# Kernel optimization log

Measured on AMD Instinct MI355X. Metric: run time of the kernel, lower is better.

## Reference

```python
import jax, jax.numpy as jnp
import numpy as np

# MoEFeedForward from ViziMarketTransformer (h100_moe_preset dims), eval mode (dropout = identity).
D, F, E, K = 512, 2048, 8, 2   # d_model, d_ff, n_experts, top_k
B, T = 8, 4096
AUX_W = 0.01


def setup_inputs() -> dict:
    key = jax.random.key(0)
    k0, k1, k2, k3 = jax.random.split(key, 4)
    s_in = 1.0 / np.sqrt(D)
    s_mid = 1.0 / np.sqrt(F)
    return {
        "x": jax.random.normal(k0, (B, T, D), jnp.float32),
        "router_w": (jax.random.normal(k1, (D, E), jnp.float32) * s_in),   # nn.Linear(d_model, n_experts, bias=False)
        "w1": (jax.random.normal(k2, (E, D, F), jnp.float32) * s_in),      # per-expert Linear(d_model, d_ff)
        "b1": jnp.zeros((E, F), jnp.float32),
        "w2": (jax.random.normal(k3, (E, F, D), jnp.float32) * s_mid),     # per-expert Linear(d_ff, d_model)
        "b2": jnp.zeros((E, D), jnp.float32),
    }


def reference(x, router_w, w1, b1, w2, b2):
    Bb, Tt, Dd = x.shape
    xf = x.reshape(-1, Dd)                                   # (N, D), N = B*T
    logits = xf @ router_w                                   # (N, E)
    topk_vals, topk_idx = jax.lax.top_k(logits, K)           # (N, K)
    topk_w = jax.nn.softmax(topk_vals, axis=-1)              # (N, K)
    # Combine weights per expert: sum over k of softmax weight where topk_idx == e.
    comb = jnp.sum(jax.nn.one_hot(topk_idx, E, dtype=xf.dtype) * topk_w[..., None], axis=1)  # (N, E)
    out = jnp.zeros_like(xf)
    for e in range(E):  # small fixed expert count; tokens fully vectorized
        h = jax.nn.gelu(xf @ w1[e] + b1[e], approximate=False)   # exact GELU, as nn.GELU()
        out = out + comb[:, e:e + 1] * (h @ w2[e] + b2[e])
    # Switch/GShard auxiliary load-balancing loss.
    probs = jax.nn.softmax(logits, axis=-1)
    avg_prob = probs.mean(axis=0)                             # (E,)
    avg_frac = jax.nn.one_hot(topk_idx[:, 0], E, dtype=xf.dtype).mean(axis=0)  # (E,)
    aux_loss = AUX_W * E * jnp.sum(avg_prob * avg_frac)
    return out.reshape(Bb, Tt, Dd), aux_loss
```

## Files before the change

### kernel.cpp

```cpp
#include <hip/hip_runtime.h>
#include <hip/hip_fp16.h>
#include <cstdint>
#include <cstddef>

#define NTOK 32768
#define DM 512
#define FF 2048
#define NE 8
#define BM 128
#define FBLK 128
#define NFB (FF / FBLK)

typedef _Float16 half8 __attribute__((ext_vector_type(8)));
typedef float floatx4 __attribute__((ext_vector_type(4)));

#define LGKM0_BARRIER() do { \
  asm volatile("s_waitcnt lgkmcnt(0)" ::: "memory"); \
  __builtin_amdgcn_s_barrier(); \
} while (0)

__global__ __launch_bounds__(256) void k_transpose(const float* __restrict__ W,
                                                   _Float16* __restrict__ Wt, int R, int C) {
  __shared__ float tile[32][33];
  int e = blockIdx.z;
  int c0 = blockIdx.x * 32, r0 = blockIdx.y * 32;
  const float* Wp = W + (size_t)e * R * C;
  _Float16* Wtp = Wt + (size_t)e * R * C;
  int tx = threadIdx.x & 31, ty = threadIdx.x >> 5;
  #pragma unroll
  for (int rr = ty; rr < 32; rr += 8)
    tile[rr][tx] = Wp[(size_t)(r0 + rr) * C + c0 + tx];
  __syncthreads();
  #pragma unroll
  for (int cc = ty; cc < 32; cc += 8)
    Wtp[(size_t)(c0 + cc) * R + r0 + tx] = (_Float16)tile[tx][cc];
}

__global__ __launch_bounds__(256) void k_router(
    const float* __restrict__ x, const float* __restrict__ rw,
    _Float16* __restrict__ xb, int* __restrict__ route_e, float* __restrict__ route_w,
    int* __restrict__ counts, float* __restrict__ aux_acc) {
  __shared__ float s_p[NE];
  __shared__ float s_c[NE];
  __shared__ int s_cnt[NE];
  int tid = threadIdx.x, lane = tid & 63, wave = tid >> 6;
  if (tid < NE) { s_p[tid] = 0.f; s_c[tid] = 0.f; s_cnt[tid] = 0; }
  __syncthreads();
  int n = blockIdx.x * 4 + wave;
  const float4* xr = (const float4*)(x + (size_t)n * DM + lane * 8);
  float4 x0 = xr[0], x1 = xr[1];
  float xv[8] = {x0.x, x0.y, x0.z, x0.w, x1.x, x1.y, x1.z, x1.w};
  float acc[NE];
  #pragma unroll
  for (int e = 0; e < NE; e++) acc[e] = 0.f;
  const float4* rwv = (const float4*)rw;
  #pragma unroll
  for (int j = 0; j < 8; j++) {
    int d = lane * 8 + j;
    float4 r0 = rwv[d * 2], r1 = rwv[d * 2 + 1];
    float xd = xv[j];
    acc[0] += xd * r0.x; acc[1] += xd * r0.y; acc[2] += xd * r0.z; acc[3] += xd * r0.w;
    acc[4] += xd * r1.x; acc[5] += xd * r1.y; acc[6] += xd * r1.z; acc[7] += xd * r1.w;
  }
  half8 hv;
  #pragma unroll
  for (int j = 0; j < 8; j++) hv[j] = (_Float16)xv[j];
  *(half8*)(xb + (size_t)n * DM + lane * 8) = hv;
  #pragma unroll
  for (int e = 0; e < NE; e++) {
    #pragma unroll
    for (int m = 1; m < 64; m <<= 1) acc[e] += __shfl_xor(acc[e], m);
  }
  if (lane == 0) {
    int e0 = 0; float v0 = acc[0];
    for (int e = 1; e < NE; e++) if (acc[e] > v0) { v0 = acc[e]; e0 = e; }
    int e1 = (e0 == 0) ? 1 : 0; float v1 = acc[e1];
    for (int e = 0; e < NE; e++) if (e != e0 && acc[e] > v1) { v1 = acc[e]; e1 = e; }
    float w0 = 1.f / (1.f + expf(v1 - v0));
    float w1 = 1.f - w0;
    route_e[n] = e0 | (e1 << 8);
    route_w[2 * n] = w0; route_w[2 * n + 1] = w1;
    float mx = acc[0];
    for (int e = 1; e < NE; e++) mx = fmaxf(mx, acc[e]);
    float p[NE]; float s = 0.f;
    for (int e = 0; e < NE; e++) { p[e] = expf(acc[e] - mx); s += p[e]; }
    float inv = 1.f / s;
    atomicAdd(&s_cnt[e0], 1); atomicAdd(&s_cnt[e1], 1);
    for (int e = 0; e < NE; e++) atomicAdd(&s_p[e], p[e] * inv);
    atomicAdd(&s_c[e0], 1.f);
  }
  __syncthreads();
  if (tid < NE) {
    atomicAdd(&counts[tid], s_cnt[tid]);
    atomicAdd(&aux_acc[tid], s_p[tid]);
    atomicAdd(&aux_acc[NE + tid], s_c[tid]);
  }
}

__global__ void k_finalize(const int* __restrict__ counts, int* __restrict__ offsets,
                           int* __restrict__ cursors, const float* __restrict__ aux_acc,
                           float* __restrict__ out_aux) {
  if (threadIdx.x == 0 && blockIdx.x == 0) {
    int off = 0;
    for (int e = 0; e < NE; e++) { offsets[e] = off; cursors[e] = off; off += counts[e]; }
    const float invN = 1.f / (float)NTOK;
    float aux = 0.f;
    for (int e = 0; e < NE; e++) aux += (aux_acc[e] * invN) * (aux_acc[NE + e] * invN);
    out_aux[0] = 0.01f * (float)NE * aux;
  }
}

__global__ __launch_bounds__(256) void k_build(
    const int* __restrict__ route_e, const float* __restrict__ route_w,
    int* __restrict__ cursors, int* __restrict__ tok, float* __restrict__ wgt,
    int* __restrict__ pos) {
  __shared__ int s_cnt[NE];
  __shared__ int s_base[NE];
  int tid = threadIdx.x;
  if (tid < NE) s_cnt[tid] = 0;
  __syncthreads();
  int n = blockIdx.x * 256 + tid;
  int re = route_e[n];
  int e0 = re & 0xff, e1 = (re >> 8) & 0xff;
  float w0 = route_w[2 * n], w1 = route_w[2 * n + 1];
  int p0 = atomicAdd(&s_cnt[e0], 1);
  int p1 = atomicAdd(&s_cnt[e1], 1);
  __syncthreads();
  if (tid < NE) s_base[tid] = atomicAdd(&cursors[tid], s_cnt[tid]);
  __syncthreads();
  int g0 = s_base[e0] + p0, g1 = s_base[e1] + p1;
  tok[g0] = n; wgt[g0] = w0; pos[n] = g0;
  tok[g1] = n; wgt[g1] = w1; pos[NTOK + n] = g1;
}

__global__ __launch_bounds__(512, 2) void k_fused(
    const _Float16* __restrict__ xb, const _Float16* __restrict__ w1t,
    const _Float16* __restrict__ w2t, const float* __restrict__ b1,
    const float* __restrict__ b2, const int* __restrict__ counts,
    const int* __restrict__ offsets, const int* __restrict__ tok,
    const float* __restrict__ wgt, _Float16* __restrict__ yb) {
  int bid = blockIdx.x;
  int e = bid & 7;
  int tm = bid >> 3;
  int cnt = counts[e];
  if (tm * BM >= cnt) return;
  int off = offsets[e];

  __shared__ _Float16 Xs[2][BM * 32];
  __shared__ _Float16 W1s[2][FBLK * 32];
  __shared__ _Float16 Hs[BM * FBLK];
  __shared__ _Float16 W2s[2][DM * 32];

  int tid = threadIdx.x, lane = tid & 63, wave = tid >> 6;
  int wr = wave >> 2, wc = wave & 3;
  int fr = lane & 15, kf = (lane >> 4) * 8;
  int rowL = tid >> 2, kc = (tid & 3) * 8;
  int rq = (lane >> 4) * 4, cq = lane & 15;

  int tr = tm * BM + rowL;
  int t0 = tok[off + (tr < cnt ? tr : 0)];
  const _Float16* ax = xb + (size_t)t0 * DM + kc;
  const _Float16* w1e = w1t + (size_t)e * FF * DM;
  const _Float16* w2e = w2t + (size_t)e * DM * FF;
  const _Float16* w2p = w2e + (size_t)rowL * FF + kc;

  floatx4 acc[4][8];
  floatx4 zero = {0.f, 0.f, 0.f, 0.f};
  #pragma unroll
  for (int i = 0; i < 4; i++)
    #pragma unroll
    for (int j = 0; j < 8; j++) acc[i][j] = zero;

  #pragma unroll 1
  for (int fb = 0; fb < NFB; fb++) {
    int fbase = fb * FBLK;
    floatx4 acc1[4][2];
    #pragma unroll
    for (int i = 0; i < 4; i++)
      #pragma unroll
      for (int j = 0; j < 2; j++) acc1[i][j] = zero;
    const _Float16* w1p = w1e + (size_t)(fbase + rowL) * DM + kc;
    half8 ra = *(const half8*)(ax);
    half8 rb = *(const half8*)(w1p);
    *(half8*)(&Xs[0][rowL * 32 + kc]) = ra;
    *(half8*)(&W1s[0][rowL * 32 + kc]) = rb;
    ra = *(const half8*)(ax + 32);
    rb = *(const half8*)(w1p + 32);
    LGKM0_BARRIER();
    #pragma unroll
    for (int k = 0; k < 16; k++) {
      int cur = k & 1, nxt = cur ^ 1;
      if (k + 1 < 16) {
        *(half8*)(&Xs[nxt][rowL * 32 + kc]) = ra;
        *(half8*)(&W1s[nxt][rowL * 32 + kc]) = rb;
      }
      if (k + 2 < 16) {
        ra = *(const half8*)(ax + (k + 2) * 32);
        rb = *(const half8*)(w1p + (k + 2) * 32);
      }
      const _Float16* Ab = &Xs[cur][(wr * 64 + fr) * 32 + kf];
      const _Float16* Bb = &W1s[cur][(wc * 32 + fr) * 32 + kf];
      half8 av[4], bv[2];
      #pragma unroll
      for (int i = 0; i < 4; i++) av[i] = *(const half8*)(Ab + i * 512);
      #pragma unroll
      for (int j = 0; j < 2; j++) bv[j] = *(const half8*)(Bb + j * 512);
      #pragma unroll
      for (int i = 0; i < 4; i++)
        #pragma unroll
        for (int j = 0; j < 2; j++)
          acc1[i][j] = __builtin_amdgcn_mfma_f32_16x16x32_f16(av[i], bv[j], acc1[i][j], 0, 0, 0);
      if (k + 1 < 16) LGKM0_BARRIER();
    }
    #pragma unroll
    for (int j = 0; j < 2; j++) {
      int col = wc * 32 + j * 16 + cq;
      float bb = b1[e * FF + fbase + col];
      #pragma unroll
      for (int i = 0; i < 4; i++) {
        #pragma unroll
        for (int r = 0; r < 4; r++) {
          int row = wr * 64 + i * 16 + rq + r;
          float v = acc1[i][j][r] + bb;
          v = 0.5f * v * (1.f + erff(v * 0.70710678118654752f));
          Hs[row * FBLK + (col ^ ((row & 7) << 3))] = (_Float16)v;
        }
      }
    }
    const _Float16* w2q = w2p + fbase;
    half8 rw0 = *(const half8*)(w2q);
    half8 rw1 = *(const half8*)(w2q + (size_t)128 * FF);
    half8 rw2 = *(const half8*)(w2q + (size_t)256 * FF);
    half8 rw3 = *(const half8*)(w2q + (size_t)384 * FF);
    *(half8*)(&W2s[0][rowL * 32 + kc]) = rw0;
    *(half8*)(&W2s[0][(rowL + 128) * 32 + kc]) = rw1;
    *(half8*)(&W2s[0][(rowL + 256) * 32 + kc]) = rw2;
    *(half8*)(&W2s[0][(rowL + 384) * 32 + kc]) = rw3;
    rw0 = *(const half8*)(w2q + 32);
    rw1 = *(const half8*)(w2q + (size_t)128 * FF + 32);
    rw2 = *(const half8*)(w2q + (size_t)256 * FF + 32);
    rw3 = *(const half8*)(w2q + (size_t)384 * FF + 32);
    LGKM0_BARRIER();
    #pragma unroll
    for (int k = 0; k < 4; k++) {
      int cur = k & 1, nxt = cur ^ 1;
      if (k + 1 < 4) {
        *(half8*)(&W2s[nxt][rowL * 32 + kc]) = rw0;
        *(half8*)(&W2s[nxt][(rowL + 128) * 32 + kc]) = rw1;
        *(half8*)(&W2s[nxt][(rowL + 256) * 32 + kc]) = rw2;
        *(half8*)(&W2s[nxt][(rowL + 384) * 32 + kc]) = rw3;
      }
      if (k + 2 < 4) {
        const _Float16* p = w2q + (k + 2) * 32;
        rw0 = *(const half8*)(p);
        rw1 = *(const half8*)(p + (size_t)128 * FF);
        rw2 = *(const half8*)(p + (size_t)256 * FF);
        rw3 = *(const half8*)(p + (size_t)384 * FF);
      }
      half8 av[4], bv[8];
      #pragma unroll
      for (int i = 0; i < 4; i++) {
        int row = wr * 64 + i * 16 + fr;
        int col = k * 32 + kf;
        av[i] = *(const half8*)(&Hs[row * FBLK + (col ^ ((row & 7) << 3))]);
      }
      #pragma unroll
      for (int j = 0; j < 8; j++)
        bv[j] = *(const half8*)(&W2s[cur][(wc * 128 + j * 16 + fr) * 32 + kf]);
      #pragma unroll
      for (int i = 0; i < 4; i++)
        #pragma unroll
        for (int j = 0; j < 8; j++)
          acc[i][j] = __builtin_amdgcn_mfma_f32_16x16x32_f16(av[i], bv[j], acc[i][j], 0, 0, 0);
      if (k + 1 < 4) LGKM0_BARRIER();
    }
  }
  float bcol[8];
  #pragma unroll
  for (int j = 0; j < 8; j++) bcol[j] = b2[e * DM + wc * 128 + j * 16 + cq];
  #pragma unroll
  for (int i = 0; i < 4; i++) {
    #pragma unroll
    for (int r = 0; r < 4; r++) {
      int row = tm * BM + wr * 64 + i * 16 + rq + r;
      if (row < cnt) {
        float w = wgt[off + row];
        _Float16* yr = yb + (size_t)(off + row) * DM + wc * 128 + cq;
        #pragma unroll
        for (int j = 0; j < 8; j++)
          yr[j * 16] = (_Float16)(w * (acc[i][j][r] + bcol[j]));
      }
    }
  }
}

__global__ __launch_bounds__(256) void k_combine(
    const _Float16* __restrict__ yb, const int* __restrict__ pos,
    float* __restrict__ out) {
  int tid = threadIdx.x, lane = tid & 63, wave = tid >> 6;
  int n = blockIdx.x * 4 + wave;
  int p0 = pos[n], p1 = pos[NTOK + n];
  half8 a = *(const half8*)(yb + (size_t)p0 * DM + lane * 8);
  half8 b = *(const half8*)(yb + (size_t)p1 * DM + lane * 8);
  float4 o0, o1;
  o0.x = (float)a[0] + (float)b[0];
  o0.y = (float)a[1] + (float)b[1];
  o0.z = (float)a[2] + (float)b[2];
  o0.w = (float)a[3] + (float)b[3];
  o1.x = (float)a[4] + (float)b[4];
  o1.y = (float)a[5] + (float)b[5];
  o1.z = (float)a[6] + (float)b[6];
  o1.w = (float)a[7] + (float)b[7];
  float4* op = (float4*)(out + (size_t)n * DM + lane * 8);
  op[0] = o0; op[1] = o1;
}

extern "C" void kernel_launch(void* const* d_in, const int* in_sizes, int n_in,
                              void* d_out, int out_size, void* d_ws, size_t ws_size,
                              hipStream_t stream) {
  const float* x  = (const float*)d_in[0];
  const float* rw = (const float*)d_in[1];
  const float* w1 = (const float*)d_in[2];
  const float* b1 = (const float*)d_in[3];
  const float* w2 = (const float*)d_in[4];
  const float* b2 = (const float*)d_in[5];
  float* out = (float*)d_out;

  uint8_t* ws = (uint8_t*)d_ws;
  _Float16* xb  = (_Float16*)ws;  ws += (size_t)NTOK * DM * 2;
  _Float16* w1t = (_Float16*)ws;  ws += (size_t)NE * FF * DM * 2;
  _Float16* w2t = (_Float16*)ws;  ws += (size_t)NE * DM * FF * 2;
  int*   tok     = (int*)ws;      ws += (size_t)2 * NTOK * 4;
  float* wgt     = (float*)ws;    ws += (size_t)2 * NTOK * 4;
  int*   pos     = (int*)ws;      ws += (size_t)2 * NTOK * 4;
  int*   route_e = (int*)ws;      ws += (size_t)NTOK * 4;
  float* route_w = (float*)ws;    ws += (size_t)NTOK * 8;
  int*   counts  = (int*)ws;      ws += 8 * 4;
  int*   offsets = (int*)ws;      ws += 8 * 4;
  int*   cursors = (int*)ws;      ws += 8 * 4;
  float* aux     = (float*)ws;    ws += 16 * 4;
  _Float16* yb  = (_Float16*)ws;

  hipMemsetAsync(counts, 0, (8 + 8 + 8 + 16) * 4, stream);

  k_transpose<<<dim3(FF / 32, DM / 32, NE), 256, 0, stream>>>(w1, w1t, DM, FF);
  k_transpose<<<dim3(DM / 32, FF / 32, NE), 256, 0, stream>>>(w2, w2t, FF, DM);
  k_router<<<NTOK / 4, 256, 0, stream>>>(x, rw, xb, route_e, route_w, counts, aux);
  k_finalize<<<1, 64, 0, stream>>>(counts, offsets, cursors, aux, out + (size_t)NTOK * DM);
  k_build<<<NTOK / 256, 256, 0, stream>>>(route_e, route_w, cursors, tok, wgt, pos);
  k_fused<<<(NTOK / BM) * NE, 512, 0, stream>>>(
      xb, w1t, w2t, b1, b2, counts, offsets, tok, wgt, yb);
  k_combine<<<NTOK / 4, 256, 0, stream>>>(yb, pos, out);
}
```

Measured before the change: 989.0 us.

## Use 1024-thread blocks with padded LDS and direct-from-global W2 fragments

The fused MoE expert kernel moves to 16 waves per block. Half the threads stage X and half stage W1, and both use padded LDS strides instead of the XOR swizzle. The second GEMM no longer stages W2 through shared memory: each wave loads its B fragments straight from global into registers, prefetched one k-step ahead, and raises wave priority around the MFMA block. This cuts the per-wave accumulator tile and LDS footprint to improve occupancy and drop the W2 LDS round trip, but every wave now loads W2 from global separately, which may raise global/L2 traffic.

```diff
diff --git a/kernel.cpp b/kernel.cpp
--- a/kernel.cpp
+++ b/kernel.cpp
@@ -10,6 +10,9 @@
 #define BM 128
 #define FBLK 128
 #define NFB (FF / FBLK)
+#define XS_STRIDE 40
+#define HS_STRIDE 136
+#define SBUF (BM * XS_STRIDE)
 
 typedef _Float16 half8 __attribute__((ext_vector_type(8)));
 typedef float floatx4 __attribute__((ext_vector_type(4)));
@@ -133,7 +136,7 @@
   tok[g1] = n; wgt[g1] = w1; pos[NTOK + n] = g1;
 }
 
-__global__ __launch_bounds__(512, 2) void k_fused(
+__global__ __launch_bounds__(1024, 4) void k_fused(
     const _Float16* __restrict__ xb, const _Float16* __restrict__ w1t,
     const _Float16* __restrict__ w2t, const float* __restrict__ b1,
     const float* __restrict__ b2, const int* __restrict__ counts,
@@ -146,148 +149,119 @@
   if (tm * BM >= cnt) return;
   int off = offsets[e];
 
-  __shared__ _Float16 Xs[2][BM * 32];
-  __shared__ _Float16 W1s[2][FBLK * 32];
-  __shared__ _Float16 Hs[BM * FBLK];
-  __shared__ _Float16 W2s[2][DM * 32];
+  __shared__ _Float16 Xs[2][SBUF];
+  __shared__ _Float16 W1s[2][SBUF];
+  __shared__ _Float16 Hs[BM * HS_STRIDE];
 
   int tid = threadIdx.x, lane = tid & 63, wave = tid >> 6;
-  int wr = wave >> 2, wc = wave & 3;
+  int wrA = wave >> 2, wcA = wave & 3;
+  int wrB = wave >> 3, wcB = wave & 7;
   int fr = lane & 15, kf = (lane >> 4) * 8;
-  int rowL = tid >> 2, kc = (tid & 3) * 8;
   int rq = (lane >> 4) * 4, cq = lane & 15;
 
+  int stx = (tid < 512);
+  int st = tid & 511;
+  int rowL = st >> 2, kc = (st & 3) * 8;
   int tr = tm * BM + rowL;
   int t0 = tok[off + (tr < cnt ? tr : 0)];
-  const _Float16* ax = xb + (size_t)t0 * DM + kc;
+  const _Float16* gx = xb + (size_t)t0 * DM + kc;
   const _Float16* w1e = w1t + (size_t)e * FF * DM;
   const _Float16* w2e = w2t + (size_t)e * DM * FF;
-  const _Float16* w2p = w2e + (size_t)rowL * FF + kc;
-
-  floatx4 acc[4][8];
+  _Float16* sdst = (stx ? &Xs[0][0] : &W1s[0][0]) + rowL * XS_STRIDE + kc;
+  const _Float16* w2base = w2e + (size_t)(wcB * 64 + fr) * FF + kf;
+
+  floatx4 acc[4][4];
   floatx4 zero = {0.f, 0.f, 0.f, 0.f};
   #pragma unroll
   for (int i = 0; i < 4; i++)
     #pragma unroll
-    for (int j = 0; j < 8; j++) acc[i][j] = zero;
+    for (int j = 0; j < 4; j++) acc[i][j] = zero;
 
   #pragma unroll 1
   for (int fb = 0; fb < NFB; fb++) {
     int fbase = fb * FBLK;
-    floatx4 acc1[4][2];
-    #pragma unroll
-    for (int i = 0; i < 4; i++)
-      #pragma unroll
-      for (int j = 0; j < 2; j++) acc1[i][j] = zero;
-    const _Float16* w1p = w1e + (size_t)(fbase + rowL) * DM + kc;
-    half8 ra = *(const half8*)(ax);
-    half8 rb = *(const half8*)(w1p);
-    *(half8*)(&Xs[0][rowL * 32 + kc]) = ra;
-    *(half8*)(&W1s[0][rowL * 32 + kc]) = rb;
-    ra = *(const half8*)(ax + 32);
-    rb = *(const half8*)(w1p + 32);
+    floatx4 acc1[2][2];
+    acc1[0][0] = zero; acc1[0][1] = zero; acc1[1][0] = zero; acc1[1][1] = zero;
+    const _Float16* asrc = stx ? gx : (w1e + (size_t)(fbase + rowL) * DM + kc);
+    half8 rs = *(const half8*)(asrc);
+    *(half8*)(sdst) = rs;
+    rs = *(const half8*)(asrc + 32);
     LGKM0_BARRIER();
     #pragma unroll
     for (int k = 0; k < 16; k++) {
-      int cur = k & 1, nxt = cur ^ 1;
-      if (k + 1 < 16) {
-        *(half8*)(&Xs[nxt][rowL * 32 + kc]) = ra;
-        *(half8*)(&W1s[nxt][rowL * 32 + kc]) = rb;
+      int cur = k & 1;
+      if (k + 1 < 16) *(half8*)(sdst + (cur ^ 1) * SBUF) = rs;
+      if (k + 2 < 16) rs = *(const half8*)(asrc + (k + 2) * 32);
+      const _Float16* Ab = &Xs[cur][(wrA * 32 + fr) * XS_STRIDE + kf];
+      const _Float16* Bb = &W1s[cur][(wcA * 32 + fr) * XS_STRIDE + kf];
+      half8 a0 = *(const half8*)(Ab);
+      half8 a1 = *(const half8*)(Ab + 16 * XS_STRIDE);
+      half8 b0 = *(const half8*)(Bb);
+      half8 b1v = *(const half8*)(Bb + 16 * XS_STRIDE);
+      acc1[0][0] = __builtin_amdgcn_mfma_f32_16x16x32_f16(a0, b0, acc1[0][0], 0, 0, 0);
+      acc1[0][1] = __builtin_amdgcn_mfma_f32_16x16x32_f16(a0, b1v, acc1[0][1], 0, 0, 0);
+      acc1[1][0] = __builtin_amdgcn_mfma_f32_16x16x32_f16(a1, b0, acc1[1][0], 0, 0, 0);
+      acc1[1][1] = __builtin_amdgcn_mfma_f32_16x16x32_f16(a1, b1v, acc1[1][1], 0, 0, 0);
+      if (k + 1 < 16) LGKM0_BARRIER();
+    }
+    half8 bvn[4];
+    {
+      const _Float16* p = w2base + fbase;
+      #pragma unroll
+      for (int j = 0; j < 4; j++) bvn[j] = *(const half8*)(p + (size_t)(j * 16) * FF);
+    }
+    #pragma unroll
+    for (int j = 0; j < 2; j++) {
+      int col = wcA * 32 + j * 16 + cq;
+      float bb = b1[e * FF + fbase + col];
+      #pragma unroll
+      for (int i = 0; i < 2; i++) {
+        int row0 = wrA * 32 + i * 16 + rq;
+        #pragma unroll
+        for (int r = 0; r < 4; r++) {
+          float v = acc1[i][j][r] + bb;
+          v = 0.5f * v * (1.f + erff(v * 0.70710678118654752f));
+          Hs[(row0 + r) * HS_STRIDE + col] = (_Float16)v;
+        }
       }
-      if (k + 2 < 16) {
-        ra = *(const half8*)(ax + (k + 2) * 32);
-        rb = *(const half8*)(w1p + (k + 2) * 32);
+    }
+    LGKM0_BARRIER();
+    #pragma unroll
+    for (int k = 0; k < 4; k++) {
+      half8 bv[4];
+      #pragma unroll
+      for (int j = 0; j < 4; j++) bv[j] = bvn[j];
+      if (k + 1 < 4) {
+        const _Float16* p = w2base + fbase + (k + 1) * 32;
+        #pragma unroll
+        for (int j = 0; j < 4; j++) bvn[j] = *(const half8*)(p + (size_t)(j * 16) * FF);
       }
-      const _Float16* Ab = &Xs[cur][(wr * 64 + fr) * 32 + kf];
-      const _Float16* Bb = &W1s[cur][(wc * 32 + fr) * 32 + kf];
-      half8 av[4], bv[2];
-      #pragma unroll
-      for (int i = 0; i < 4; i++) av[i] = *(const half8*)(Ab + i * 512);
-      #pragma unroll
-      for (int j = 0; j < 2; j++) bv[j] = *(const half8*)(Bb + j * 512);
+      half8 av[4];
+      #pragma unroll
+      for (int i = 0; i < 4; i++)
+        av[i] = *(const half8*)(&Hs[(wrB * 64 + i * 16 + fr) * HS_STRIDE + k * 32 + kf]);
+      __builtin_amdgcn_s_setprio(1);
       #pragma unroll
       for (int i = 0; i < 4; i++)
         #pragma unroll
-        for (int j = 0; j < 2; j++)
-          acc1[i][j] = __builtin_amdgcn_mfma_f32_16x16x32_f16(av[i], bv[j], acc1[i][j], 0, 0, 0);
-      if (k + 1 < 16) LGKM0_BARRIER();
-    }
-    #pragma unroll
-    for (int j = 0; j < 2; j++) {
-      int col = wc * 32 + j * 16 + cq;
-      float bb = b1[e * FF + fbase + col];
-      #pragma unroll
-      for (int i = 0; i < 4; i++) {
-        #pragma unroll
-        for (int r = 0; r < 4; r++) {
-          int row = wr * 64 + i * 16 + rq + r;
-          float v = acc1[i][j][r] + bb;
-          v = 0.5f * v * (1.f + erff(v * 0.70710678118654752f));
-          Hs[row * FBLK + (col ^ ((row & 7) << 3))] = (_Float16)v;
-        }
-      }
-    }
-    const _Float16* w2q = w2p + fbase;
-    half8 rw0 = *(const half8*)(w2q);
-    half8 rw1 = *(const half8*)(w2q + (size_t)128 * FF);
-    half8 rw2 = *(const half8*)(w2q + (size_t)256 * FF);
-    half8 rw3 = *(const half8*)(w2q + (size_t)384 * FF);
-    *(half8*)(&W2s[0][rowL * 32 + kc]) = rw0;
-    *(half8*)(&W2s[0][(rowL + 128) * 32 + kc]) = rw1;
-    *(half8*)(&W2s[0][(rowL + 256) * 32 + kc]) = rw2;
-    *(half8*)(&W2s[0][(rowL + 384) * 32 + kc]) = rw3;
-    rw0 = *(const half8*)(w2q + 32);
-    rw1 = *(const half8*)(w2q + (size_t)128 * FF + 32);
-    rw2 = *(const half8*)(w2q + (size_t)256 * FF + 32);
-    rw3 = *(const half8*)(w2q + (size_t)384 * FF + 32);
-    LGKM0_BARRIER();
-    #pragma unroll
-    for (int k = 0; k < 4; k++) {
-      int cur = k & 1, nxt = cur ^ 1;
-      if (k + 1 < 4) {
-        *(half8*)(&W2s[nxt][rowL * 32 + kc]) = rw0;
-        *(half8*)(&W2s[nxt][(rowL + 128) * 32 + kc]) = rw1;
-        *(half8*)(&W2s[nxt][(rowL + 256) * 32 + kc]) = rw2;
-        *(half8*)(&W2s[nxt][(rowL + 384) * 32 + kc]) = rw3;
-      }
-      if (k + 2 < 4) {
-        const _Float16* p = w2q + (k + 2) * 32;
-        rw0 = *(const half8*)(p);
-        rw1 = *(const half8*)(p + (size_t)128 * FF);
-        rw2 = *(const half8*)(p + (size_t)256 * FF);
-        rw3 = *(const half8*)(p + (size_t)384 * FF);
-      }
-      half8 av[4], bv[8];
-      #pragma unroll
-      for (int i = 0; i < 4; i++) {
-        int row = wr * 64 + i * 16 + fr;
-        int col = k * 32 + kf;
-        av[i] = *(const half8*)(&Hs[row * FBLK + (col ^ ((row & 7) << 3))]);
-      }
-      #pragma unroll
-      for (int j = 0; j < 8; j++)
-        bv[j] = *(const half8*)(&W2s[cur][(wc * 128 + j * 16 + fr) * 32 + kf]);
-      #pragma unroll
-      for (int i = 0; i < 4; i++)
-        #pragma unroll
-        for (int j = 0; j < 8; j++)
+        for (int j = 0; j < 4; j++)
           acc[i][j] = __builtin_amdgcn_mfma_f32_16x16x32_f16(av[i], bv[j], acc[i][j], 0, 0, 0);
-      if (k + 1 < 4) LGKM0_BARRIER();
-    }
-  }
-  float bcol[8];
-  #pragma unroll
-  for (int j = 0; j < 8; j++) bcol[j] = b2[e * DM + wc * 128 + j * 16 + cq];
+      __builtin_amdgcn_s_setprio(0);
+    }
+  }
+  float bcol[4];
+  #pragma unroll
+  for (int j = 0; j < 4; j++) bcol[j] = b2[e * DM + wcB * 64 + j * 16 + cq];
   #pragma unroll
   for (int i = 0; i < 4; i++) {
     #pragma unroll
     for (int r = 0; r < 4; r++) {
-      int row = tm * BM + wr * 64 + i * 16 + rq + r;
+      int row = tm * BM + wrB * 64 + i * 16 + rq + r;
       if (row < cnt) {
         float w = wgt[off + row];
-        _Float16* yr = yb + (size_t)(off + row) * DM + wc * 128 + cq;
+        _Float16* yr = yb + (size_t)(off + row) * DM + wcB * 64 + cq;
         #pragma unroll
-        for (int j = 0; j < 8; j++)
+        for (int j = 0; j < 4; j++)
           yr[j * 16] = (_Float16)(w * (acc[i][j][r] + bcol[j]));
       }
     }
@@ -348,7 +322,7 @@
   k_router<<<NTOK / 4, 256, 0, stream>>>(x, rw, xb, route_e, route_w, counts, aux);
   k_finalize<<<1, 64, 0, stream>>>(counts, offsets, cursors, aux, out + (size_t)NTOK * DM);
   k_build<<<NTOK / 256, 256, 0, stream>>>(route_e, route_w, cursors, tok, wgt, pos);
-  k_fused<<<(NTOK / BM) * NE, 512, 0, stream>>>(
+  k_fused<<<(NTOK / BM) * NE, 1024, 0, stream>>>(
       xb, w1t, w2t, b1, b2, counts, offsets, tok, wgt, yb);
   k_combine<<<NTOK / 4, 256, 0, stream>>>(yb, pos, out);
 }
```

Result: slower. 1.207 ms (+22.0%).
